# Kernel tuning notes

Hardware: AMD Instinct MI355X
Metric: run time of the kernel (lower is better)

## Reference

```python
import jax, jax.numpy as jnp
import numpy as np

B, T, D = 8, 1024, 512
V = 8192  # codebook_size


def setup_inputs() -> dict:
    key = jax.random.key(0)
    k1, k2, k3 = jax.random.split(key, 3)
    scale_w = float(np.sqrt(2.0 / (D + V)))  # xavier_uniform-ish scale
    scale_c = float(np.sqrt(2.0 / (V + D)))
    return {
        "inputs": jax.random.normal(k1, (B, T, D), dtype=jnp.float32),
        "codebook": jax.random.normal(k2, (V, D), dtype=jnp.float32) * scale_c,
        "W_logits": jax.random.normal(k3, (V, D), dtype=jnp.float32) * scale_w,
        "b_logits": jnp.zeros((V,), dtype=jnp.float32),
    }


def reference(inputs, codebook, W_logits, b_logits):
    # logits = Linear(input_dim -> codebook_size)
    logits = jnp.einsum("btd,vd->btv", inputs, W_logits) + b_logits  # [B,T,V]
    # eval mode: no gumbel noise, no temperature division
    soft_tokens = jax.nn.softmax(logits, axis=-1)
    token_indices = jnp.argmax(soft_tokens, axis=-1)  # [B,T]
    hard_tokens = jax.nn.one_hot(token_indices, codebook.shape[0], dtype=soft_tokens.dtype)
    # straight-through: hard values, soft gradients
    tokens_for_lookup = soft_tokens + jax.lax.stop_gradient(hard_tokens - soft_tokens)
    quantized = jnp.einsum("btv,vd->btd", tokens_for_lookup, codebook)  # [B,T,D]
    commitment_loss = jnp.mean((quantized - jax.lax.stop_gradient(inputs)) ** 2)
    return quantized, token_indices, commitment_loss, soft_tokens, logits
```

## Files before the change

### kernel.cpp

```cpp
#include <hip/hip_runtime.h>
#include <hip/hip_bf16.h>

#define BT_ 8192
#define D_  512
#define V_  8192
#define NT2 32

#define OFF_Q      0
#define OFF_TOK    4194304
#define OFF_LOSS   4202496
#define OFF_SOFT   4202497
#define OFF_LOGITS 71311361
#define STAGE_F    4202500

#define TAU  0.02f

typedef __attribute__((ext_vector_type(8))) short bf16x8;
typedef __attribute__((ext_vector_type(4))) float f32x4;
typedef __attribute__((ext_vector_type(4))) unsigned short u16x4;

__device__ __forceinline__ unsigned short bf16rne(float f) {
  unsigned int u = __float_as_uint(f);
  return (unsigned short)((u + 0x7fffu + ((u >> 16) & 1u)) >> 16);
}

__global__ __launch_bounds__(256) void to_bf16_k(const float4* __restrict__ x,
                                                 const float4* __restrict__ w,
                                                 u16x4* __restrict__ xa,
                                                 u16x4* __restrict__ wb) {
  const int n4 = (BT_ * D_) / 4;
  const int half = gridDim.x >> 1;
  const bool isw = blockIdx.x >= half;
  const float4* __restrict__ s = isw ? w : x;
  u16x4* __restrict__ d = isw ? wb : xa;
  const int b0 = isw ? blockIdx.x - half : blockIdx.x;
  for (int i = b0 * 256 + threadIdx.x; i < n4; i += half * 256) {
    const float4 v = s[i];
    u16x4 o;
    o[0] = bf16rne(v.x); o[1] = bf16rne(v.y);
    o[2] = bf16rne(v.z); o[3] = bf16rne(v.w);
    d[i] = o;
  }
}

__device__ __forceinline__ void gload_lds16(const void* g, void* l) {
  __builtin_amdgcn_global_load_lds((const __attribute__((address_space(1))) void*)g,
                                   (__attribute__((address_space(3))) void*)l,
                                   16, 0, 0);
}

__device__ __forceinline__ void barf() {
  __builtin_amdgcn_s_barrier();
  asm volatile("" ::: "memory");
}
__device__ __forceinline__ void vmcnt2() { asm volatile("s_waitcnt vmcnt(2)" ::: "memory"); }
__device__ __forceinline__ void vmcnt0() { asm volatile("s_waitcnt vmcnt(0)" ::: "memory"); }

__device__ __forceinline__ void stage_unit(const char* __restrict__ tb, char* ldsRegion,
                                           int ktile, int half, int wid, int lane) {
#pragma unroll
  for (int issue = 0; issue < 2; ++issue) {
    const int d = half * 16384 + issue * 8192 + wid * 1024 + lane * 16;
    const int l = d ^ (((d >> 7) & 7) << 4);
    gload_lds16(tb + (size_t)(l >> 7) * 1024 + ktile * 128 + (l & 127),
                ldsRegion + half * 16384 + issue * 8192 + wid * 1024);
  }
}

__device__ __forceinline__ bf16x8 rdfrag(const char* base, int R, int ks, int g) {
  return *(const bf16x8*)(base + R * 128 + ((ks * 64 + 16 * g) ^ ((R & 7) << 4)));
}

__device__ __forceinline__ void kgroup(int t, int smode, char* lds,
                                       const char* __restrict__ Ab,
                                       const char* __restrict__ Bb,
                                       int wr, int wc, int lane, int wid,
                                       f32x4 (&acc)[8][4]) {
  char* aL = lds + (t & 1) * 32768;
  char* bL = lds + 65536 + (t & 1) * 32768;
  char* aS = lds + ((t & 1) ^ 1) * 32768;
  char* bS = lds + 65536 + ((t & 1) ^ 1) * 32768;
  const int cg = lane & 15, g = lane >> 4;
  bf16x8 a[4][2], b0[2][2], b1[2][2];

#pragma unroll
  for (int m = 0; m < 4; ++m)
#pragma unroll
    for (int ks = 0; ks < 2; ++ks)
      a[m][ks] = rdfrag(aL, wr * 128 + m * 16 + cg, ks, g);
#pragma unroll
  for (int n = 0; n < 2; ++n)
#pragma unroll
    for (int ks = 0; ks < 2; ++ks)
      b0[n][ks] = rdfrag(bL, wc * 64 + n * 16 + cg, ks, g);
  if (smode >= 1) stage_unit(Ab, aS, t + 1, 1, wid, lane);
  barf();
  __builtin_amdgcn_s_setprio(1);
#pragma unroll
  for (int m = 0; m < 4; ++m)
#pragma unroll
    for (int n = 0; n < 2; ++n)
#pragma unroll
      for (int ks = 0; ks < 2; ++ks)
        acc[m][n] = __builtin_amdgcn_mfma_f32_16x16x32_bf16(a[m][ks], b0[n][ks], acc[m][n], 0, 0, 0);
  __builtin_amdgcn_s_setprio(0);
  barf();

#pragma unroll
  for (int n = 0; n < 2; ++n)
#pragma unroll
    for (int ks = 0; ks < 2; ++ks)
      b1[n][ks] = rdfrag(bL, wc * 64 + (n + 2) * 16 + cg, ks, g);
  if (smode >= 1) stage_unit(Bb, bS, t + 1, 0, wid, lane);
  barf();
  __builtin_amdgcn_s_setprio(1);
#pragma unroll
  for (int m = 0; m < 4; ++m)
#pragma unroll
    for (int n = 0; n < 2; ++n)
#pragma unroll
      for (int ks = 0; ks < 2; ++ks)
        acc[m][n + 2] = __builtin_amdgcn_mfma_f32_16x16x32_bf16(a[m][ks], b1[n][ks], acc[m][n + 2], 0, 0, 0);
  __builtin_amdgcn_s_setprio(0);
  barf();

#pragma unroll
  for (int m = 0; m < 4; ++m)
#pragma unroll
    for (int ks = 0; ks < 2; ++ks)
      a[m][ks] = rdfrag(aL, wr * 128 + (m + 4) * 16 + cg, ks, g);
  if (smode >= 1) stage_unit(Bb, bS, t + 1, 1, wid, lane);
  barf();
  __builtin_amdgcn_s_setprio(1);
#pragma unroll
  for (int m = 0; m < 4; ++m)
#pragma unroll
    for (int n = 0; n < 2; ++n)
#pragma unroll
      for (int ks = 0; ks < 2; ++ks)
        acc[m + 4][n + 2] = __builtin_amdgcn_mfma_f32_16x16x32_bf16(a[m][ks], b1[n][ks], acc[m + 4][n + 2], 0, 0, 0);
  __builtin_amdgcn_s_setprio(0);
  barf();

  if (smode == 2) stage_unit(Ab, aL, t + 2, 0, wid, lane);
  barf();
  __builtin_amdgcn_s_setprio(1);
#pragma unroll
  for (int m = 0; m < 4; ++m)
#pragma unroll
    for (int n = 0; n < 2; ++n)
#pragma unroll
      for (int ks = 0; ks < 2; ++ks)
        acc[m + 4][n] = __builtin_amdgcn_mfma_f32_16x16x32_bf16(a[m][ks], b0[n][ks], acc[m + 4][n], 0, 0, 0);
  __builtin_amdgcn_s_setprio(0);
  if (smode == 2) vmcnt2();
  else if (smode == 1) vmcnt0();
  barf();
}

__global__ __launch_bounds__(512, 2) void gemm8(const unsigned short* __restrict__ A,
                                                const unsigned short* __restrict__ B,
                                                const float* __restrict__ bias,
                                                float* __restrict__ C,
                                                float* __restrict__ pmaxT,
                                                float* __restrict__ psumT) {
  __shared__ char lds[131072];
  const int tid  = threadIdx.x;
  const int lane = tid & 63;
  const int wid  = tid >> 6;
  const int wr   = wid >> 2, wc = wid & 3;

  const int bid = blockIdx.x;
  const int xcd = bid & 7;
  const int s   = bid >> 3;
  const int by  = (xcd >> 1) * 8 + (s >> 4);
  const int bx  = (xcd & 1) * 16 + (s & 15);
  const int row0 = by * 256, col0 = bx * 256;

  const char* Ab = (const char*)A + (size_t)row0 * 1024;
  const char* Bb = (const char*)B + (size_t)col0 * 1024;

  f32x4 acc[8][4] = {};

  stage_unit(Ab, lds, 0, 0, wid, lane);
  stage_unit(Ab, lds, 0, 1, wid, lane);
  stage_unit(Bb, lds + 65536, 0, 0, wid, lane);
  stage_unit(Bb, lds + 65536, 0, 1, wid, lane);
  stage_unit(Ab, lds + 32768, 1, 0, wid, lane);
  vmcnt2();
  barf();

  for (int t = 0; t < 6; ++t)
    kgroup(t, 2, lds, Ab, Bb, wr, wc, lane, wid, acc);
  kgroup(6, 1, lds, Ab, Bb, wr, wc, lane, wid, acc);
  kgroup(7, 0, lds, Ab, Bb, wr, wc, lane, wid, acc);

  float* pmS = (float*)lds;
  float* psS = (float*)lds + 1024;
  const int cg = lane & 15, g = lane >> 4;

  float bv[4];
#pragma unroll
  for (int n = 0; n < 4; ++n) bv[n] = bias[col0 + wc * 64 + n * 16 + cg];

#pragma unroll
  for (int m = 0; m < 8; ++m) {
#pragma unroll
    for (int rr = 0; rr < 4; ++rr) {
      const int R = wr * 128 + m * 16 + 4 * g + rr;
      const size_t rowg = row0 + R;
      float vmx = -1e30f, vsm = 0.f;
#pragma unroll
      for (int n = 0; n < 4; ++n) {
        const float v = acc[m][n][rr] + bv[n];
        C[rowg * V_ + col0 + wc * 64 + n * 16 + cg] = v;
        vmx = fmaxf(vmx, v);
        vsm += __expf(v);
      }
#pragma unroll
      for (int o = 1; o < 16; o <<= 1) {
        vmx = fmaxf(vmx, __shfl_xor(vmx, o));
        vsm += __shfl_xor(vsm, o);
      }
      if (cg == 0) { pmS[wc * 256 + R] = vmx; psS[wc * 256 + R] = vsm; }
    }
  }
  __syncthreads();
  if (tid < 256) {
    float mx = fmaxf(fmaxf(pmS[tid], pmS[256 + tid]), fmaxf(pmS[512 + tid], pmS[768 + tid]));
    float sm = psS[tid] + psS[256 + tid] + psS[512 + tid] + psS[768 + tid];
    pmaxT[(size_t)bx * BT_ + row0 + tid] = mx;
    psumT[(size_t)bx * BT_ + row0 + tid] = sm;
  }
}

__global__ __launch_bounds__(256) void row_finish(const float* __restrict__ logits,
                                                  const float* __restrict__ pmaxT,
                                                  const float* __restrict__ psumT,
                                                  const float* __restrict__ xf,
                                                  const float* __restrict__ wf,
                                                  const float* __restrict__ bias,
                                                  float* __restrict__ tokf,
                                                  float* __restrict__ soft) {
  const int row  = blockIdx.x;
  const int tid  = threadIdx.x;
  const int lane = tid & 63;
  const int wv   = tid >> 6;

  const int tl = lane & 31;
  const float pm = pmaxT[(size_t)tl * BT_ + row];
  const float ps = psumT[(size_t)tl * BT_ + row];
  float m = pm, s = ps;
#pragma unroll
  for (int o = 1; o < 32; o <<= 1) {
    m = fmaxf(m, __shfl_xor(m, o));
    s += __shfl_xor(s, o);
  }
  const float si = 1.0f / s;

  const float* L = logits + (size_t)row * V_;
  float*       S = soft   + (size_t)row * V_;
  const float4* L4 = (const float4*)(L + 3);
  float4*       S4 = (float4*)(S + 3);

  if (wv == 0) {
    const float thr = m - TAU;
    unsigned long long tmask = __ballot(pm >= thr) & 0xFFFFFFFFull;
    float bestv = -1e30f;
    int   besti = 0x7fffffff;
    const float4* xr4 = (const float4*)(xf + (size_t)row * D_);
    while (tmask) {
      const int t = __ffsll(tmask) - 1;
      tmask &= tmask - 1;
      const float* Lr = L + t * 256;
#pragma unroll
      for (int kq = 0; kq < 4; ++kq) {
        const float lv = Lr[kq * 64 + lane];
        unsigned long long c = __ballot(lv >= thr);
        while (c) {
          const int j = __ffsll(c) - 1;
          c &= c - 1;
          const int col = t * 256 + kq * 64 + j;
          const float4* wr4 = (const float4*)(wf + (size_t)col * D_);
          float p = 0.f;
#pragma unroll
          for (int q = 0; q < 2; ++q) {
            const float4 av = xr4[lane + 64 * q];
            const float4 bvv = wr4[lane + 64 * q];
            p += av.x * bvv.x + av.y * bvv.y + av.z * bvv.z + av.w * bvv.w;
          }
#pragma unroll
          for (int o = 1; o < 64; o <<= 1) p += __shfl_xor(p, o);
          const float tot = p + bias[col];
          if (tot > bestv || (tot == bestv && col < besti)) { bestv = tot; besti = col; }
        }
      }
    }
    if (lane == 0) tokf[row] = (float)besti;
    if (lane < 3)  S[lane] = __expf(L[lane]) * si;
    if (lane == 3) S[8191] = __expf(L[8191]) * si;
#pragma unroll
    for (int k = 0; k < 2; ++k) {
      const int i = 1920 + k * 64 + lane;
      if (i < 2047) {
        const float4 v = L4[i];
        float4 o;
        o.x = __expf(v.x) * si; o.y = __expf(v.y) * si;
        o.z = __expf(v.z) * si; o.w = __expf(v.w) * si;
        S4[i] = o;
      }
    }
  } else {
    const int t = tid - 64;
#pragma unroll
    for (int k = 0; k < 10; ++k) {
      const int i = k * 192 + t;
      const float4 v = L4[i];
      float4 o;
      o.x = __expf(v.x) * si; o.y = __expf(v.y) * si;
      o.z = __expf(v.z) * si; o.w = __expf(v.w) * si;
      S4[i] = o;
    }
  }
}

__global__ __launch_bounds__(256) void finalize_k(const float* __restrict__ tokf,
                                                  const float* __restrict__ cb,
                                                  const float* __restrict__ xf,
                                                  float* __restrict__ q,
                                                  float* __restrict__ loss) {
  const int row  = blockIdx.x * 4 + (threadIdx.x >> 6);
  const int lane = threadIdx.x & 63;
  const int idx  = (int)tokf[row];
  const float4* cr = (const float4*)(cb + (size_t)idx * D_);
  const float4* xr = (const float4*)(xf + (size_t)row * D_);
  float4* qr = (float4*)(q + (size_t)row * D_);
  float ls = 0.f;
#pragma unroll
  for (int j = 0; j < 2; ++j) {
    const int c = lane + j * 64;
    const float4 cv = cr[c];
    const float4 xv = xr[c];
    qr[c] = cv;
    const float dx = cv.x - xv.x, dy = cv.y - xv.y, dz = cv.z - xv.z, dw = cv.w - xv.w;
    ls += dx * dx + dy * dy + dz * dz + dw * dw;
  }
#pragma unroll
  for (int o = 32; o; o >>= 1) ls += __shfl_xor(ls, o);
  if (lane == 0) atomicAdd(loss, ls * (1.0f / 4194304.0f));
}

extern "C" void kernel_launch(void* const* d_in, const int* in_sizes, int n_in,
                              void* d_out, int out_size, void* d_ws, size_t ws_size,
                              hipStream_t stream) {
  const float* x  = (const float*)d_in[0];
  const float* cb = (const float*)d_in[1];
  const float* wl = (const float*)d_in[2];
  const float* bl = (const float*)d_in[3];
  float* out = (float*)d_out;

  float* qout   = out + OFF_Q;
  float* tokf   = out + OFF_TOK;
  float* loss   = out + OFF_LOSS;
  float* soft   = out + OFF_SOFT;
  float* logits = out + OFF_LOGITS;

  unsigned short* Abf = (unsigned short*)(out + STAGE_F);
  unsigned short* Wbf = Abf + (size_t)BT_ * D_;
  float* pmaxT = qout;
  float* psumT = qout + 262144;

  hipMemsetAsync(loss, 0, 4, stream);

  to_bf16_k<<<2048, 256, 0, stream>>>((const float4*)x, (const float4*)wl,
                                      (u16x4*)Abf, (u16x4*)Wbf);
  gemm8<<<1024, 512, 0, stream>>>(Abf, Wbf, bl, logits, pmaxT, psumT);
  row_finish<<<8192, 256, 0, stream>>>(logits, pmaxT, psumT, x, wl, bl, tokf, soft);
  finalize_k<<<2048, 256, 0, stream>>>(tokf, cb, x, qout, loss);
}
```

Baseline: 373.0 us.

## Stage GEMM epilogue through LDS for coalesced nontemporal logits stores

The GEMM epilogue now writes the accumulator tile into LDS in two halves, then each wave reads full rows back to emit coalesced 16-byte nontemporal stores of logits. Row max and sum are computed per row with a wave-wide reduction instead of partial LDS reductions. Nontemporal loads and stores are added across the bf16 conversion, softmax and finalize kernels to avoid polluting cache with streamed data. The 2-blocks-per-CU launch bound is dropped, and the added LDS round trip and barriers cost extra time in exchange for wider store transactions.

```diff
diff --git a/kernel.cpp b/kernel.cpp
--- a/kernel.cpp
+++ b/kernel.cpp
@@ -24,21 +24,21 @@
   return (unsigned short)((u + 0x7fffu + ((u >> 16) & 1u)) >> 16);
 }
 
-__global__ __launch_bounds__(256) void to_bf16_k(const float4* __restrict__ x,
-                                                 const float4* __restrict__ w,
+__global__ __launch_bounds__(256) void to_bf16_k(const f32x4* __restrict__ x,
+                                                 const f32x4* __restrict__ w,
                                                  u16x4* __restrict__ xa,
                                                  u16x4* __restrict__ wb) {
   const int n4 = (BT_ * D_) / 4;
   const int half = gridDim.x >> 1;
   const bool isw = blockIdx.x >= half;
-  const float4* __restrict__ s = isw ? w : x;
+  const f32x4* __restrict__ s = isw ? w : x;
   u16x4* __restrict__ d = isw ? wb : xa;
   const int b0 = isw ? blockIdx.x - half : blockIdx.x;
   for (int i = b0 * 256 + threadIdx.x; i < n4; i += half * 256) {
-    const float4 v = s[i];
+    const f32x4 v = __builtin_nontemporal_load(s + i);
     u16x4 o;
-    o[0] = bf16rne(v.x); o[1] = bf16rne(v.y);
-    o[2] = bf16rne(v.z); o[3] = bf16rne(v.w);
+    o[0] = bf16rne(v[0]); o[1] = bf16rne(v[1]);
+    o[2] = bf16rne(v[2]); o[3] = bf16rne(v[3]);
     d[i] = o;
   }
 }
@@ -158,12 +158,12 @@
   barf();
 }
 
-__global__ __launch_bounds__(512, 2) void gemm8(const unsigned short* __restrict__ A,
-                                                const unsigned short* __restrict__ B,
-                                                const float* __restrict__ bias,
-                                                float* __restrict__ C,
-                                                float* __restrict__ pmaxT,
-                                                float* __restrict__ psumT) {
+__global__ __launch_bounds__(512) void gemm8(const unsigned short* __restrict__ A,
+                                             const unsigned short* __restrict__ B,
+                                             const float* __restrict__ bias,
+                                             float* __restrict__ C,
+                                             float* __restrict__ pmaxT,
+                                             float* __restrict__ psumT) {
   __shared__ char lds[131072];
   const int tid  = threadIdx.x;
   const int lane = tid & 63;
@@ -195,42 +195,56 @@
   kgroup(6, 1, lds, Ab, Bb, wr, wc, lane, wid, acc);
   kgroup(7, 0, lds, Ab, Bb, wr, wc, lane, wid, acc);
 
-  float* pmS = (float*)lds;
-  float* psS = (float*)lds + 1024;
   const int cg = lane & 15, g = lane >> 4;
-
   float bv[4];
 #pragma unroll
   for (int n = 0; n < 4; ++n) bv[n] = bias[col0 + wc * 64 + n * 16 + cg];
 
-#pragma unroll
-  for (int m = 0; m < 8; ++m) {
-#pragma unroll
-    for (int rr = 0; rr < 4; ++rr) {
-      const int R = wr * 128 + m * 16 + 4 * g + rr;
-      const size_t rowg = row0 + R;
-      float vmx = -1e30f, vsm = 0.f;
-#pragma unroll
-      for (int n = 0; n < 4; ++n) {
-        const float v = acc[m][n][rr] + bv[n];
-        C[rowg * V_ + col0 + wc * 64 + n * 16 + cg] = v;
-        vmx = fmaxf(vmx, v);
-        vsm += __expf(v);
-      }
-#pragma unroll
-      for (int o = 1; o < 16; o <<= 1) {
+  float* cl = (float*)lds;
+  __syncthreads();
+#pragma unroll
+  for (int h = 0; h < 2; ++h) {
+    if (wr == h) {
+#pragma unroll
+      for (int m = 0; m < 8; ++m)
+#pragma unroll
+        for (int n = 0; n < 4; ++n) {
+          const int cw = ((wc * 64 + n * 16 + cg) + 253) & 255;
+#pragma unroll
+          for (int rr = 0; rr < 4; ++rr) {
+            const int R = m * 16 + 4 * g + rr;
+            cl[R * 256 + cw] = acc[m][n][rr] + bv[n];
+          }
+        }
+    }
+    __syncthreads();
+#pragma unroll
+    for (int k = 0; k < 16; ++k) {
+      const int r = wid * 16 + k;
+      const f32x4 v = *(const f32x4*)((char*)cl + r * 1024 + lane * 16);
+      float vmx = fmaxf(fmaxf(v[0], v[1]), fmaxf(v[2], v[3]));
+      float vsm = __expf(v[0]) + __expf(v[1]) + __expf(v[2]) + __expf(v[3]);
+#pragma unroll
+      for (int o = 1; o < 64; o <<= 1) {
         vmx = fmaxf(vmx, __shfl_xor(vmx, o));
         vsm += __shfl_xor(vsm, o);
       }
-      if (cg == 0) { pmS[wc * 256 + R] = vmx; psS[wc * 256 + R] = vsm; }
-    }
-  }
-  __syncthreads();
-  if (tid < 256) {
-    float mx = fmaxf(fmaxf(pmS[tid], pmS[256 + tid]), fmaxf(pmS[512 + tid], pmS[768 + tid]));
-    float sm = psS[tid] + psS[256 + tid] + psS[512 + tid] + psS[768 + tid];
-    pmaxT[(size_t)bx * BT_ + row0 + tid] = mx;
-    psumT[(size_t)bx * BT_ + row0 + tid] = sm;
+      const int grow = row0 + h * 128 + r;
+      float* Crow = C + (size_t)grow * V_ + col0;
+      if (lane < 63) {
+        __builtin_nontemporal_store(v, (f32x4*)(Crow + 3) + lane);
+      } else {
+        __builtin_nontemporal_store(v[0], Crow + 255);
+        __builtin_nontemporal_store(v[1], Crow + 0);
+        __builtin_nontemporal_store(v[2], Crow + 1);
+        __builtin_nontemporal_store(v[3], Crow + 2);
+      }
+      if (lane == 0) {
+        pmaxT[(size_t)bx * BT_ + grow] = vmx;
+        psumT[(size_t)bx * BT_ + grow] = vsm;
+      }
+    }
+    __syncthreads();
   }
 }
 
@@ -260,8 +274,8 @@
 
   const float* L = logits + (size_t)row * V_;
   float*       S = soft   + (size_t)row * V_;
-  const float4* L4 = (const float4*)(L + 3);
-  float4*       S4 = (float4*)(S + 3);
+  const f32x4* L4 = (const f32x4*)(L + 3);
+  f32x4*       S4 = (f32x4*)(S + 3);
 
   if (wv == 0) {
     const float thr = m - TAU;
@@ -303,11 +317,11 @@
     for (int k = 0; k < 2; ++k) {
       const int i = 1920 + k * 64 + lane;
       if (i < 2047) {
-        const float4 v = L4[i];
-        float4 o;
-        o.x = __expf(v.x) * si; o.y = __expf(v.y) * si;
-        o.z = __expf(v.z) * si; o.w = __expf(v.w) * si;
-        S4[i] = o;
+        const f32x4 v = __builtin_nontemporal_load(L4 + i);
+        f32x4 o;
+        o[0] = __expf(v[0]) * si; o[1] = __expf(v[1]) * si;
+        o[2] = __expf(v[2]) * si; o[3] = __expf(v[3]) * si;
+        __builtin_nontemporal_store(o, S4 + i);
       }
     }
   } else {
@@ -315,11 +329,11 @@
 #pragma unroll
     for (int k = 0; k < 10; ++k) {
       const int i = k * 192 + t;
-      const float4 v = L4[i];
-      float4 o;
-      o.x = __expf(v.x) * si; o.y = __expf(v.y) * si;
-      o.z = __expf(v.z) * si; o.w = __expf(v.w) * si;
-      S4[i] = o;
+      const f32x4 v = __builtin_nontemporal_load(L4 + i);
+      f32x4 o;
+      o[0] = __expf(v[0]) * si; o[1] = __expf(v[1]) * si;
+      o[2] = __expf(v[2]) * si; o[3] = __expf(v[3]) * si;
+      __builtin_nontemporal_store(o, S4 + i);
     }
   }
 }
@@ -332,17 +346,17 @@
   const int row  = blockIdx.x * 4 + (threadIdx.x >> 6);
   const int lane = threadIdx.x & 63;
   const int idx  = (int)tokf[row];
-  const float4* cr = (const float4*)(cb + (size_t)idx * D_);
-  const float4* xr = (const float4*)(xf + (size_t)row * D_);
-  float4* qr = (float4*)(q + (size_t)row * D_);
+  const f32x4* cr = (const f32x4*)(cb + (size_t)idx * D_);
+  const f32x4* xr = (const f32x4*)(xf + (size_t)row * D_);
+  f32x4* qr = (f32x4*)(q + (size_t)row * D_);
   float ls = 0.f;
 #pragma unroll
   for (int j = 0; j < 2; ++j) {
     const int c = lane + j * 64;
-    const float4 cv = cr[c];
-    const float4 xv = xr[c];
-    qr[c] = cv;
-    const float dx = cv.x - xv.x, dy = cv.y - xv.y, dz = cv.z - xv.z, dw = cv.w - xv.w;
+    const f32x4 cv = cr[c];
+    const f32x4 xv = __builtin_nontemporal_load(xr + c);
+    __builtin_nontemporal_store(cv, qr + c);
+    const float dx = cv[0] - xv[0], dy = cv[1] - xv[1], dz = cv[2] - xv[2], dw = cv[3] - xv[3];
     ls += dx * dx + dy * dy + dz * dz + dw * dw;
   }
 #pragma unroll
@@ -372,7 +386,7 @@
 
   hipMemsetAsync(loss, 0, 4, stream);
 
-  to_bf16_k<<<2048, 256, 0, stream>>>((const float4*)x, (const float4*)wl,
+  to_bf16_k<<<2048, 256, 0, stream>>>((const f32x4*)x, (const f32x4*)wl,
                                       (u16x4*)Abf, (u16x4*)Wbf);
   gemm8<<<1024, 512, 0, stream>>>(Abf, Wbf, bl, logits, pmaxT, psumT);
   row_finish<<<8192, 256, 0, stream>>>(logits, pmaxT, psumT, x, wl, bl, tokf, soft);
```

Result: slower. 382.7 us (+2.6%).
